# Kernel optimization log

Hardware: AMD Instinct MI355X
Metric: run time of the kernel (lower is better)

## Reference

```python
import jax, jax.numpy as jnp
import numpy as np

N_EMBD = 2048
N_EXPERTS = 8
MOE_LOSS_COEFF = 0.01


def setup_inputs() -> dict:
    key = jax.random.key(0)
    kx, kw = jax.random.split(key)
    x = jax.random.normal(kx, (4, 4096, N_EMBD), dtype=jnp.float32)
    # nn.Linear(n_embd, n_experts, bias=False): weight [n_experts, n_embd]
    bound = 1.0 / np.sqrt(N_EMBD)
    W = jax.random.uniform(kw, (N_EXPERTS, N_EMBD), dtype=jnp.float32,
                           minval=-bound, maxval=bound)
    return {"x": x, "W": W}


def reference(x, W):
    n_experts = W.shape[0]
    # gate linear: logits [B, T, E]
    logits = jnp.einsum("btd,ed->bte", x, W)
    probs = jax.nn.softmax(logits, axis=-1)
    # top-2 selection and renormalization
    top2_vals, top2_idx = jax.lax.top_k(probs, 2)  # [B,T,2]
    gate_probs_top2 = top2_vals / jnp.sum(top2_vals, axis=-1, keepdims=True)
    # aux load-balancing loss stats
    importance = jnp.mean(probs, axis=(0, 1))  # [E]
    top1_idx = jnp.argmax(probs, axis=-1)      # [B,T]
    one_hot = jax.nn.one_hot(top1_idx, n_experts, dtype=jnp.float32)
    load = jnp.mean(one_hot, axis=(0, 1))      # [E]
    aux_loss = n_experts * jnp.sum(importance * load) * MOE_LOSS_COEFF
    return gate_probs_top2, top2_idx, aux_loss
```

## Files before the change

kernel.cpp:

```cpp
#include <hip/hip_runtime.h>

#define NEMBD 2048
#define ROW4 (NEMBD / 4)
#define CHUNKS (ROW4 / 64)
#define NEXP 8
#define W4N (NEXP * ROW4)

__global__ __launch_bounds__(1024) void gate_kernel(
    const float* __restrict__ x, const float* __restrict__ W,
    float* __restrict__ out, float* __restrict__ ws, int ntok)
{
    __shared__ float4 Wl[W4N];

    const int tid  = threadIdx.x;
    const int lane = tid & 63;
    const int wid  = tid >> 6;

    const float4* X4 = (const float4*)x;
    const float4* W4 = (const float4*)W;

    #pragma unroll
    for (int k = 0; k < 4; ++k)
        Wl[tid + k * 1024] = W4[tid + k * 1024];
    __syncthreads();

    const int t0 = blockIdx.x * 32 + wid * 2;
    const bool va0 = t0 < ntok, va1 = (t0 + 1) < ntok;

    float* out_p = out;
    float* out_i = out + 2 * ntok;

    float a[16];
    #pragma unroll
    for (int q = 0; q < 16; ++q) a[q] = 0.f;

    const float4 z4 = make_float4(0.f, 0.f, 0.f, 0.f);

    #pragma unroll 2
    for (int i = 0; i < CHUNKS; ++i) {
        const int col = i * 64 + lane;
        float4 x0 = va0 ? X4[(size_t)t0 * ROW4 + col] : z4;
        float4 x1 = va1 ? X4[(size_t)(t0 + 1) * ROW4 + col] : z4;
        #pragma unroll
        for (int e = 0; e < 8; ++e) {
            float4 wv = Wl[e * ROW4 + col];
            a[e]     += x0.x * wv.x + x0.y * wv.y + x0.z * wv.z + x0.w * wv.w;
            a[8 + e] += x1.x * wv.x + x1.y * wv.y + x1.z * wv.z + x1.w * wv.w;
        }
    }

    #pragma unroll
    for (int q = 0; q < 16; ++q) a[q] += __shfl_xor(a[q], 32, 64);
    #pragma unroll
    for (int q = 0; q < 16; ++q) a[q] += __shfl_xor(a[q], 16, 64);
    #pragma unroll
    for (int s = 0; s < 4; ++s) {
        const int hm = 8 >> s;
        const bool hi = (lane & hm) != 0;
        #pragma unroll
        for (int q = 0; q < 8; ++q) {
            if (q < hm) {
                float send = hi ? a[q] : a[q + hm];
                float recv = __shfl_xor(send, hm, 64);
                float keep = hi ? a[q + hm] : a[q];
                a[q] = keep + recv;
            }
        }
    }
    const float logit = a[0];
    const int e = lane & 7;
    const int k = (lane >> 3) & 1;
    const bool tvalid = (t0 + k) < ntok;

    float m = logit;
    #pragma unroll
    for (int mm = 1; mm <= 4; mm <<= 1) m = fmaxf(m, __shfl_xor(m, mm, 64));
    float p = __expf(logit - m);
    float ssum = p;
    #pragma unroll
    for (int mm = 1; mm <= 4; mm <<= 1) ssum += __shfl_xor(ssum, mm, 64);
    const float prob = p / ssum;

    float v1 = prob, v2 = -1.f;
    int   i1 = e,    i2 = -1;
    #pragma unroll
    for (int mm = 1; mm <= 4; mm <<= 1) {
        float b1 = __shfl_xor(v1, mm, 64);
        float b2 = __shfl_xor(v2, mm, 64);
        int  bi1 = __shfl_xor(i1, mm, 64);
        int  bi2 = __shfl_xor(i2, mm, 64);
        bool aw = (v1 > b1) || (v1 == b1 && i1 < bi1);
        float w1 = aw ? v1 : b1;  int wi1 = aw ? i1 : bi1;
        float l1 = aw ? b1 : v1;  int li1 = aw ? bi1 : i1;
        float w2 = aw ? v2 : b2;  int wi2 = aw ? i2 : bi2;
        bool sw = (l1 > w2) || (l1 == w2 && li1 < wi2);
        v1 = w1; i1 = wi1;
        v2 = sw ? l1 : w2;  i2 = sw ? li1 : wi2;
    }

    if (e == 0 && lane < 16 && tvalid) {
        const int t = t0 + k;
        const float denom = v1 + v2;
        out_p[2 * t]     = v1 / denom;
        out_p[2 * t + 1] = v2 / denom;
        out_i[2 * t]     = (float)i1;
        out_i[2 * t + 1] = (float)i2;
    }

    float pc = tvalid ? prob : 0.f;
    float oc = (tvalid && e == i1) ? 1.f : 0.f;
    pc += __shfl_xor(pc, 8, 64);
    oc += __shfl_xor(oc, 8, 64);

    float* part = (float*)Wl;
    __syncthreads();
    if (lane < 8)       part[wid * 16 + lane] = pc;
    else if (lane < 16) part[wid * 16 + lane] = oc;
    __syncthreads();
    if (tid < 16) {
        float v = 0.f;
        #pragma unroll
        for (int w = 0; w < 16; ++w) v += part[w * 16 + tid];
        ws[blockIdx.x * 16 + tid] = v;
    }
}

__global__ void finalize_kernel(const float* __restrict__ ws,
                                float* __restrict__ out, int nblk, int ntok)
{
    __shared__ float s[16][16];
    __shared__ float tot[16];
    const int t = threadIdx.x;
    const int slot = t & 15, chunk = t >> 4;
    float p = 0.f;
    for (int b = chunk; b < nblk; b += 16) p += ws[b * 16 + slot];
    s[chunk][slot] = p;
    __syncthreads();
    if (t < 16) {
        float v = 0.f;
        #pragma unroll
        for (int c = 0; c < 16; ++c) v += s[c][t];
        tot[t] = v;
    }
    __syncthreads();
    if (t == 0) {
        const float inv = 1.f / (float)ntok;
        float aux = 0.f;
        #pragma unroll
        for (int e = 0; e < 8; ++e)
            aux += (tot[e] * inv) * (tot[8 + e] * inv);
        out[4 * ntok] = 8.f * aux * 0.01f;
    }
}

extern "C" void kernel_launch(void* const* d_in, const int* in_sizes, int n_in,
                              void* d_out, int out_size, void* d_ws, size_t ws_size,
                              hipStream_t stream)
{
    const float* x = (const float*)d_in[0];
    const float* W = (const float*)d_in[1];
    const int ntok    = in_sizes[0] / NEMBD;
    const int nblocks = (ntok + 31) / 32;

    gate_kernel<<<nblocks, 1024, 0, stream>>>(
        x, W, (float*)d_out, (float*)d_ws, ntok);
    finalize_kernel<<<1, 256, 0, stream>>>(
        (const float*)d_ws, (float*)d_out, nblocks, ntok);
}
```

Measured before the change: 211.4 us.

## Prefetch all x rows into registers around W smem staging, use 512-thread blocks

Each wave now issues every global load for its two token rows up front, half of them before the W copy into shared memory and half after the barrier. This hides the W staging latency behind x loads. Blocks shrink from 1024 to 512 threads, which doubles the block count and the number of times W is copied to shared memory. The loads now held in registers raise register pressure and can lower occupancy.

Result: slower. 286.1 us (+35.3%).

```diff
diff --git a/kernel.cpp b/kernel.cpp
--- a/kernel.cpp
+++ b/kernel.cpp
@@ -2,11 +2,10 @@
 
 #define NEMBD 2048
 #define ROW4 (NEMBD / 4)
-#define CHUNKS (ROW4 / 64)
 #define NEXP 8
 #define W4N (NEXP * ROW4)
 
-__global__ __launch_bounds__(1024) void gate_kernel(
+__global__ __launch_bounds__(512) void gate_kernel(
     const float* __restrict__ x, const float* __restrict__ W,
     float* __restrict__ out, float* __restrict__ ws, int ntok)
 {
@@ -19,33 +18,57 @@
     const float4* X4 = (const float4*)x;
     const float4* W4 = (const float4*)W;
 
+    const int t0 = blockIdx.x * 16 + wid * 2;
+    const bool va0 = t0 < ntok, va1 = (t0 + 1) < ntok;
+    const float4 z4 = make_float4(0.f, 0.f, 0.f, 0.f);
+
+    float4 xa0[4], xa1[4];
     #pragma unroll
-    for (int k = 0; k < 4; ++k)
-        Wl[tid + k * 1024] = W4[tid + k * 1024];
+    for (int i = 0; i < 4; ++i) {
+        const int col = i * 64 + lane;
+        xa0[i] = va0 ? X4[(size_t)t0 * ROW4 + col] : z4;
+        xa1[i] = va1 ? X4[(size_t)(t0 + 1) * ROW4 + col] : z4;
+    }
+
+    #pragma unroll
+    for (int k = 0; k < 8; ++k)
+        Wl[tid + k * 512] = W4[tid + k * 512];
     __syncthreads();
 
-    const int t0 = blockIdx.x * 32 + wid * 2;
-    const bool va0 = t0 < ntok, va1 = (t0 + 1) < ntok;
-
-    float* out_p = out;
-    float* out_i = out + 2 * ntok;
+    float4 xb0[4], xb1[4];
+    #pragma unroll
+    for (int i = 0; i < 4; ++i) {
+        const int col = (i + 4) * 64 + lane;
+        xb0[i] = va0 ? X4[(size_t)t0 * ROW4 + col] : z4;
+        xb1[i] = va1 ? X4[(size_t)(t0 + 1) * ROW4 + col] : z4;
+    }
 
     float a[16];
     #pragma unroll
     for (int q = 0; q < 16; ++q) a[q] = 0.f;
 
-    const float4 z4 = make_float4(0.f, 0.f, 0.f, 0.f);
-
-    #pragma unroll 2
-    for (int i = 0; i < CHUNKS; ++i) {
+    #pragma unroll
+    for (int i = 0; i < 4; ++i) {
         const int col = i * 64 + lane;
-        float4 x0 = va0 ? X4[(size_t)t0 * ROW4 + col] : z4;
-        float4 x1 = va1 ? X4[(size_t)(t0 + 1) * ROW4 + col] : z4;
         #pragma unroll
         for (int e = 0; e < 8; ++e) {
             float4 wv = Wl[e * ROW4 + col];
-            a[e]     += x0.x * wv.x + x0.y * wv.y + x0.z * wv.z + x0.w * wv.w;
-            a[8 + e] += x1.x * wv.x + x1.y * wv.y + x1.z * wv.z + x1.w * wv.w;
+            a[e]     += xa0[i].x * wv.x + xa0[i].y * wv.y
+                      + xa0[i].z * wv.z + xa0[i].w * wv.w;
+            a[8 + e] += xa1[i].x * wv.x + xa1[i].y * wv.y
+                      + xa1[i].z * wv.z + xa1[i].w * wv.w;
+        }
+    }
+    #pragma unroll
+    for (int i = 0; i < 4; ++i) {
+        const int col = (i + 4) * 64 + lane;
+        #pragma unroll
+        for (int e = 0; e < 8; ++e) {
+            float4 wv = Wl[e * ROW4 + col];
+            a[e]     += xb0[i].x * wv.x + xb0[i].y * wv.y
+                      + xb0[i].z * wv.z + xb0[i].w * wv.w;
+            a[8 + e] += xb1[i].x * wv.x + xb1[i].y * wv.y
+                      + xb1[i].z * wv.z + xb1[i].w * wv.w;
         }
     }
 
@@ -71,6 +94,9 @@
     const int e = lane & 7;
     const int k = (lane >> 3) & 1;
     const bool tvalid = (t0 + k) < ntok;
+
+    float* out_p = out;
+    float* out_i = out + 2 * ntok;
 
     float m = logit;
     #pragma unroll
@@ -120,7 +146,7 @@
     if (tid < 16) {
         float v = 0.f;
         #pragma unroll
-        for (int w = 0; w < 16; ++w) v += part[w * 16 + tid];
+        for (int w = 0; w < 8; ++w) v += part[w * 16 + tid];
         ws[blockIdx.x * 16 + tid] = v;
     }
 }
@@ -160,9 +186,9 @@
     const float* x = (const float*)d_in[0];
     const float* W = (const float*)d_in[1];
     const int ntok    = in_sizes[0] / NEMBD;
-    const int nblocks = (ntok + 31) / 32;
+    const int nblocks = (ntok + 15) / 16;
 
-    gate_kernel<<<nblocks, 1024, 0, stream>>>(
+    gate_kernel<<<nblocks, 512, 0, stream>>>(
         x, W, (float*)d_out, (float*)d_ws, ntok);
     finalize_kernel<<<1, 256, 0, stream>>>(
         (const float*)d_ws, (float*)d_out, nblocks, ntok);
```

## Halve block size and software-pipeline x loads across two token groups per wave

Applied to the files above, without the earlier changes.

Blocks shrink to 512 threads, and each wave now handles two token pairs. Register-buffered loads of x are issued ahead of compute (double-buffered XA/XB) and separated by sched_barriers, so global latency overlaps the dot products and the W-to-LDS copy. This amortizes the 64KB shared W load over more work per thread. The cost is higher register pressure (launch bounds 512,4) and fewer waves per block to hide latency.

Result: slower. 440.5 us (+108.4%).

```diff
diff --git a/kernel.cpp b/kernel.cpp
--- a/kernel.cpp
+++ b/kernel.cpp
@@ -2,53 +2,42 @@
 
 #define NEMBD 2048
 #define ROW4 (NEMBD / 4)
-#define CHUNKS (ROW4 / 64)
 #define NEXP 8
 #define W4N (NEXP * ROW4)
 
-__global__ __launch_bounds__(1024) void gate_kernel(
-    const float* __restrict__ x, const float* __restrict__ W,
-    float* __restrict__ out, float* __restrict__ ws, int ntok)
-{
-    __shared__ float4 Wl[W4N];
-
-    const int tid  = threadIdx.x;
-    const int lane = tid & 63;
-    const int wid  = tid >> 6;
-
-    const float4* X4 = (const float4*)x;
-    const float4* W4 = (const float4*)W;
-
-    #pragma unroll
-    for (int k = 0; k < 4; ++k)
-        Wl[tid + k * 1024] = W4[tid + k * 1024];
-    __syncthreads();
-
-    const int t0 = blockIdx.x * 32 + wid * 2;
-    const bool va0 = t0 < ntok, va1 = (t0 + 1) < ntok;
-
-    float* out_p = out;
-    float* out_i = out + 2 * ntok;
-
-    float a[16];
-    #pragma unroll
-    for (int q = 0; q < 16; ++q) a[q] = 0.f;
-
+__device__ __forceinline__ float dot4(float4 a, float4 b) {
+    return a.x * b.x + a.y * b.y + a.z * b.z + a.w * b.w;
+}
+
+__device__ __forceinline__ void issue_loads(const float4* __restrict__ X4,
+        float4 (&X)[8], int t0, int h, int lane, int ntok) {
     const float4 z4 = make_float4(0.f, 0.f, 0.f, 0.f);
-
-    #pragma unroll 2
-    for (int i = 0; i < CHUNKS; ++i) {
-        const int col = i * 64 + lane;
-        float4 x0 = va0 ? X4[(size_t)t0 * ROW4 + col] : z4;
-        float4 x1 = va1 ? X4[(size_t)(t0 + 1) * ROW4 + col] : z4;
+    const bool v0 = t0 < ntok, v1 = (t0 + 1) < ntok;
+    #pragma unroll
+    for (int c = 0; c < 4; ++c) {
+        const int col = (h * 4 + c) * 64 + lane;
+        X[c]     = v0 ? X4[(size_t)t0 * ROW4 + col] : z4;
+        X[4 + c] = v1 ? X4[(size_t)(t0 + 1) * ROW4 + col] : z4;
+    }
+}
+
+__device__ __forceinline__ void compute_half(const float4* __restrict__ Wl,
+        const float4 (&X)[8], float (&a)[16], int h, int lane) {
+    #pragma unroll
+    for (int c = 0; c < 4; ++c) {
+        const int col = (h * 4 + c) * 64 + lane;
         #pragma unroll
         for (int e = 0; e < 8; ++e) {
             float4 wv = Wl[e * ROW4 + col];
-            a[e]     += x0.x * wv.x + x0.y * wv.y + x0.z * wv.z + x0.w * wv.w;
-            a[8 + e] += x1.x * wv.x + x1.y * wv.y + x1.z * wv.z + x1.w * wv.w;
+            a[e]     += dot4(X[c], wv);
+            a[8 + e] += dot4(X[4 + c], wv);
         }
     }
-
+}
+
+__device__ __forceinline__ void finish_group(float (&a)[16], int t0, int lane,
+        int ntok, float* __restrict__ out_p, float* __restrict__ out_i,
+        float& imp_acc, float& load_acc) {
     #pragma unroll
     for (int q = 0; q < 16; ++q) a[q] += __shfl_xor(a[q], 32, 64);
     #pragma unroll
@@ -111,16 +100,72 @@
     float oc = (tvalid && e == i1) ? 1.f : 0.f;
     pc += __shfl_xor(pc, 8, 64);
     oc += __shfl_xor(oc, 8, 64);
+    imp_acc  += pc;
+    load_acc += oc;
+}
+
+__global__ __launch_bounds__(512, 4) void gate_kernel(
+    const float* __restrict__ x, const float* __restrict__ W,
+    float* __restrict__ out, float* __restrict__ ws, int ntok)
+{
+    __shared__ float4 Wl[W4N];
+
+    const int tid  = threadIdx.x;
+    const int lane = tid & 63;
+    const int wid  = tid >> 6;
+
+    const float4* X4 = (const float4*)x;
+    const float4* W4 = (const float4*)W;
+    float* out_p = out;
+    float* out_i = out + 2 * ntok;
+
+    const int tb  = blockIdx.x * 32;
+    const int tg0 = tb + wid * 2;
+    const int tg1 = tb + 16 + wid * 2;
+
+    float4 XA[8], XB[8];
+    float a[16];
+    float imp_acc = 0.f, load_acc = 0.f;
+
+    issue_loads(X4, XA, tg0, 0, lane, ntok);
+    #pragma unroll
+    for (int k2 = 0; k2 < 8; ++k2)
+        Wl[tid + k2 * 512] = W4[tid + k2 * 512];
+    __syncthreads();
+
+    issue_loads(X4, XB, tg0, 1, lane, ntok);
+    __builtin_amdgcn_sched_barrier(0);
+
+    #pragma unroll
+    for (int q = 0; q < 16; ++q) a[q] = 0.f;
+    compute_half(Wl, XA, a, 0, lane);
+    __builtin_amdgcn_sched_barrier(0);
+
+    issue_loads(X4, XA, tg1, 0, lane, ntok);
+    __builtin_amdgcn_sched_barrier(0);
+
+    compute_half(Wl, XB, a, 1, lane);
+    finish_group(a, tg0, lane, ntok, out_p, out_i, imp_acc, load_acc);
+    __builtin_amdgcn_sched_barrier(0);
+
+    issue_loads(X4, XB, tg1, 1, lane, ntok);
+    __builtin_amdgcn_sched_barrier(0);
+
+    #pragma unroll
+    for (int q = 0; q < 16; ++q) a[q] = 0.f;
+    compute_half(Wl, XA, a, 0, lane);
+    compute_half(Wl, XB, a, 1, lane);
+    finish_group(a, tg1, lane, ntok, out_p, out_i, imp_acc, load_acc);
 
     float* part = (float*)Wl;
     __syncthreads();
-    if (lane < 8)       part[wid * 16 + lane] = pc;
-    else if (lane < 16) part[wid * 16 + lane] = oc;
+    if (lane < 8)       part[wid * 16 + lane] = imp_acc;
+    else if (lane < 16) part[wid * 16 + lane] = load_acc;
     __syncthreads();
     if (tid < 16) {
         float v = 0.f;
         #pragma unroll
-        for (int w = 0; w < 16; ++w) v += part[w * 16 + tid];
+        for (int w = 0; w < 8; ++w) v += part[w * 16 + tid];
         ws[blockIdx.x * 16 + tid] = v;
     }
 }
@@ -162,7 +207,7 @@
     const int ntok    = in_sizes[0] / NEMBD;
     const int nblocks = (ntok + 31) / 32;
 
-    gate_kernel<<<nblocks, 1024, 0, stream>>>(
+    gate_kernel<<<nblocks, 512, 0, stream>>>(
         x, W, (float*)d_out, (float*)d_ws, ntok);
     finalize_kernel<<<1, 256, 0, stream>>>(
         (const float*)d_ws, (float*)d_out, nblocks, ntok);
```
